# Performance work log

Measured on AMD Instinct MI355X. Metric: run time of the kernel, lower is better.

The kernel has to match this reference:

```python
import jax, jax.numpy as jnp
import numpy as np
from jax import lax

# Model dims (see init_kwargs / mamba_ssm defaults)
B_, L_, D_IN = 8, 512, 128
D_MODEL, N_LAYERS = 512, 2
EXPAND, D_STATE, D_CONV = 2, 16, 4
D_INNER = EXPAND * D_MODEL          # 1024
DT_RANK = (D_MODEL + 15) // 16      # 32


def setup_inputs() -> dict:
    key = jax.random.key(0)
    ks = iter(jax.random.split(key, 32))
    def p(shape, scale=0.02):
        return jax.random.normal(next(ks), shape, jnp.float32) * scale
    inp = {}
    inp["x"] = jax.random.normal(next(ks), (B_, L_, D_IN), jnp.float32)
    # input projection (Linear(input_dim, d_model), with bias)
    inp["proj_in_w"] = p((D_MODEL, D_IN))
    inp["proj_in_b"] = p((D_MODEL,))
    # stacked per-layer Mamba params (leading dim = N_LAYERS)
    inp["in_proj_w"] = p((N_LAYERS, 2 * D_INNER, D_MODEL))      # no bias (mamba default)
    inp["conv_w"]    = p((N_LAYERS, D_INNER, D_CONV))           # depthwise conv1d
    inp["conv_b"]    = p((N_LAYERS, D_INNER))
    inp["x_proj_w"]  = p((N_LAYERS, DT_RANK + 2 * D_STATE, D_INNER))
    inp["dt_proj_w"] = p((N_LAYERS, D_INNER, DT_RANK))
    inp["dt_proj_b"] = jnp.full((N_LAYERS, D_INNER), 0.1, jnp.float32)
    inp["A_log"]     = jnp.log(jnp.tile(jnp.arange(1, D_STATE + 1, dtype=jnp.float32), (N_LAYERS, D_INNER, 1)))
    inp["Dm"]        = jnp.ones((N_LAYERS, D_INNER), jnp.float32)
    inp["out_proj_w"] = p((N_LAYERS, D_MODEL, D_INNER))         # no bias
    # classifier head: Linear(d_model, 64) -> ReLU -> Linear(64, 1)
    inp["cls_w1"] = p((64, D_MODEL)); inp["cls_b1"] = p((64,))
    inp["cls_w2"] = p((1, 64));       inp["cls_b2"] = p((1,))
    return inp


def _mamba_block(h, in_w, cw, cb, xp_w, dt_w, dt_b, A_log, Dm, out_w):
    B, L, _ = h.shape
    xz = jnp.einsum('bld,ed->ble', h, in_w)           # (B, L, 2*d_inner)
    xi, z = jnp.split(xz, 2, axis=-1)
    # causal depthwise conv1d (pad left d_conv-1, crop to L)
    xc = xi.transpose(0, 2, 1)                         # (B, d_inner, L)
    xc = lax.conv_general_dilated(
        xc, cw[:, None, :], (1,), [(D_CONV - 1, 0)],
        feature_group_count=D_INNER,
        dimension_numbers=('NCH', 'OIH', 'NCH')) + cb[None, :, None]
    xc = jax.nn.silu(xc).transpose(0, 2, 1)            # (B, L, d_inner)
    x_dbl = jnp.einsum('bld,ed->ble', xc, xp_w)        # (B, L, dt_rank + 2*d_state)
    dt, Bm, Cm = jnp.split(x_dbl, [DT_RANK, DT_RANK + D_STATE], axis=-1)
    dt = jax.nn.softplus(jnp.einsum('blr,dr->bld', dt, dt_w) + dt_b)  # (B, L, d_inner)
    A = -jnp.exp(A_log)                                # (d_inner, d_state)

    def step(hst, ins):
        dt_t, B_t, C_t, x_t = ins                      # (B,di),(B,ds),(B,ds),(B,di)
        dA = jnp.exp(dt_t[..., None] * A)              # (B, di, ds)
        hst = dA * hst + (dt_t * x_t)[..., None] * B_t[:, None, :]
        y = jnp.einsum('bds,bs->bd', hst, C_t)
        return hst, y

    h0 = jnp.zeros((B, D_INNER, D_STATE), h.dtype)
    xs = (dt.transpose(1, 0, 2), Bm.transpose(1, 0, 2),
          Cm.transpose(1, 0, 2), xc.transpose(1, 0, 2))
    _, ys = lax.scan(step, h0, xs)                     # ys: (L, B, d_inner)
    y = ys.transpose(1, 0, 2) + xc * Dm                # skip term D*x
    y = y * jax.nn.silu(z)                             # gate
    return jnp.einsum('ble,de->bld', y, out_w)         # (B, L, d_model)


def reference(x, proj_in_w, proj_in_b, in_proj_w, conv_w, conv_b, x_proj_w,
              dt_proj_w, dt_proj_b, A_log, Dm, out_proj_w,
              cls_w1, cls_b1, cls_w2, cls_b2):
    h = jnp.einsum('bli,di->bld', x, proj_in_w) + proj_in_b
    for l in range(N_LAYERS):
        h = _mamba_block(h, in_proj_w[l], conv_w[l], conv_b[l], x_proj_w[l],
                         dt_proj_w[l], dt_proj_b[l], A_log[l], Dm[l], out_proj_w[l])
    h = h.mean(axis=1)                                 # (B, d_model); dropout = identity (eval)
    h = jax.nn.relu(h @ cls_w1.T + cls_b1)
    logits = (h @ cls_w2.T + cls_b2).squeeze(-1)       # (B,)
    return logits
```

## Files before the change

### kernel.cpp

```cpp
#include <hip/hip_runtime.h>
#include <hip/hip_bf16.h>

#define B_   8
#define L_   512
#define DIN  128
#define DM   512
#define NLAY 2
#define DI   1024
#define DS   16
#define DTR  32
#define BL   (B_ * L_)
#define KS   8
#define CL   128
#define NCH  (L_ / CL)

typedef short bf16x8 __attribute__((ext_vector_type(8)));
typedef float floatx4 __attribute__((ext_vector_type(4)));

__device__ __forceinline__ unsigned short f2bf(float f) {
    unsigned int u = __float_as_uint(f);
    unsigned int r = (u + 0x7FFF + ((u >> 16) & 1)) >> 16;
    return (unsigned short)r;
}
__device__ __forceinline__ float bf2f(unsigned short u) {
    return __uint_as_float((unsigned int)u << 16);
}

#if __has_builtin(__builtin_amdgcn_exp2f)
#define EXP2(x) __builtin_amdgcn_exp2f(x)
#else
#define EXP2(x) __expf((x) * 0.69314718056f)
#endif

__global__ __launch_bounds__(256) void cvt_all(
    const float* __restrict__ x,  unsigned short* __restrict__ xbf,
    const float* __restrict__ pw, unsigned short* __restrict__ wpin,
    const float* __restrict__ iw, unsigned short* __restrict__ win,
    const float* __restrict__ ow, unsigned short* __restrict__ wout,
    float* __restrict__ hm)
{
    int bid = blockIdx.x;
    if (bid >= 1824) {
        int i = (bid - 1824) * 2048 + threadIdx.x * 8;
        float4 z = make_float4(0.f, 0.f, 0.f, 0.f);
        *(float4*)(hm + i) = z;
        *(float4*)(hm + i + 4) = z;
        return;
    }
    const float* src; unsigned short* dst; int off;
    if      (bid < 256)  { src = x;  dst = xbf;  off = bid; }
    else if (bid < 288)  { src = pw; dst = wpin; off = bid - 256; }
    else if (bid < 1312) { src = iw; dst = win;  off = bid - 288; }
    else                 { src = ow; dst = wout; off = bid - 1312; }
    int i = (off * 256 + threadIdx.x) * 8;
    float4 a = *(const float4*)(src + i);
    float4 b = *(const float4*)(src + i + 4);
    unsigned short o[8];
    o[0] = f2bf(a.x); o[1] = f2bf(a.y); o[2] = f2bf(a.z); o[3] = f2bf(a.w);
    o[4] = f2bf(b.x); o[5] = f2bf(b.y); o[6] = f2bf(b.z); o[7] = f2bf(b.w);
    *(uint4*)(dst + i) = *(uint4*)o;
}

__global__ __launch_bounds__(256) void gemm_mfma(
    const unsigned short* __restrict__ A,
    const unsigned short* __restrict__ W,
    float* __restrict__ C, unsigned short* __restrict__ Cb,
    int N, int K)
{
    __shared__ unsigned short As[128 * 40];
    __shared__ unsigned short Ws[128 * 40];

    const int tid  = threadIdx.x;
    const int row  = tid >> 1;
    const int half = tid & 1;
    const long aBase = (long)(blockIdx.y * 128 + row) * K + half * 16;
    const long wBase = (long)(blockIdx.x * 128 + row) * K + half * 16;
    const int  lbase = row * 40 + half * 16;

    const int lane = tid & 63;
    const int wv   = tid >> 6;
    const int wm   = (wv >> 1) * 64;
    const int wn   = (wv & 1) * 64;
    const int lr   = lane & 15;
    const int q    = lane >> 4;

    floatx4 acc[4][4];
#pragma unroll
    for (int i = 0; i < 4; ++i)
#pragma unroll
        for (int j = 0; j < 4; ++j)
#pragma unroll
            for (int r = 0; r < 4; ++r) acc[i][j][r] = 0.f;

    for (int k0 = 0; k0 < K; k0 += 32) {
        __syncthreads();
        const unsigned short* ap = A + aBase + k0;
        const unsigned short* wp = W + wBase + k0;
        uint4 a0 = *(const uint4*)ap;
        uint4 a1 = *(const uint4*)(ap + 8);
        uint4 w0 = *(const uint4*)wp;
        uint4 w1 = *(const uint4*)(wp + 8);
        *(uint4*)(As + lbase)     = a0;
        *(uint4*)(As + lbase + 8) = a1;
        *(uint4*)(Ws + lbase)     = w0;
        *(uint4*)(Ws + lbase + 8) = w1;
        __syncthreads();

        bf16x8 af[4], bfr[4];
#pragma unroll
        for (int i = 0; i < 4; ++i)
            af[i] = *(const bf16x8*)(As + (wm + i * 16 + lr) * 40 + q * 8);
#pragma unroll
        for (int j = 0; j < 4; ++j)
            bfr[j] = *(const bf16x8*)(Ws + (wn + j * 16 + lr) * 40 + q * 8);
#pragma unroll
        for (int i = 0; i < 4; ++i)
#pragma unroll
            for (int j = 0; j < 4; ++j)
                acc[i][j] = __builtin_amdgcn_mfma_f32_16x16x32_bf16(
                    af[i], bfr[j], acc[i][j], 0, 0, 0);
    }

#pragma unroll
    for (int i = 0; i < 4; ++i) {
#pragma unroll
        for (int r = 0; r < 4; ++r) {
            const int  crow = blockIdx.y * 128 + wm + i * 16 + q * 4 + r;
            const long base = (long)crow * N + blockIdx.x * 128 + wn + lr;
#pragma unroll
            for (int j = 0; j < 4; ++j) {
                float v = acc[i][j][r];
                if (C)  C[base + j * 16] = v;
                if (Cb) Cb[base + j * 16] = f2bf(v);
            }
        }
    }
}

__global__ __launch_bounds__(256) void gemm_mfma_n64(
    const unsigned short* __restrict__ A,
    const unsigned short* __restrict__ W,
    const float* __restrict__ bias,
    float* __restrict__ C, unsigned short* __restrict__ Cb,
    int N, int K, int meanmode, float* __restrict__ hm)
{
    __shared__ unsigned short As[128 * 40];
    __shared__ unsigned short Ws[64 * 40];
    __shared__ float colsum[64];

    const int tid   = threadIdx.x;
    const int arow  = tid >> 1;
    const int ahalf = tid & 1;
    const long aBase = (long)(blockIdx.y * 128 + arow) * K + ahalf * 16;
    const int  albase = arow * 40 + ahalf * 16;
    const int wrow = tid >> 2;
    const int wq   = tid & 3;
    const long wBase = (long)(blockIdx.x * 64 + wrow) * K + wq * 8;
    const int  wlbase = wrow * 40 + wq * 8;

    const int lane = tid & 63;
    const int wv   = tid >> 6;
    const int wm   = wv * 32;
    const int lr   = lane & 15;
    const int q    = lane >> 4;

    floatx4 acc[2][4];
#pragma unroll
    for (int i = 0; i < 2; ++i)
#pragma unroll
        for (int j = 0; j < 4; ++j)
#pragma unroll
            for (int r = 0; r < 4; ++r) acc[i][j][r] = 0.f;

    for (int k0 = 0; k0 < K; k0 += 32) {
        __syncthreads();
        const unsigned short* ap = A + aBase + k0;
        uint4 a0 = *(const uint4*)ap;
        uint4 a1 = *(const uint4*)(ap + 8);
        uint4 w0 = *(const uint4*)(W + wBase + k0);
        *(uint4*)(As + albase)     = a0;
        *(uint4*)(As + albase + 8) = a1;
        *(uint4*)(Ws + wlbase)     = w0;
        __syncthreads();

        bf16x8 af[2], bfr[4];
#pragma unroll
        for (int i = 0; i < 2; ++i)
            af[i] = *(const bf16x8*)(As + (wm + i * 16 + lr) * 40 + q * 8);
#pragma unroll
        for (int j = 0; j < 4; ++j)
            bfr[j] = *(const bf16x8*)(Ws + (j * 16 + lr) * 40 + q * 8);
#pragma unroll
        for (int i = 0; i < 2; ++i)
#pragma unroll
            for (int j = 0; j < 4; ++j)
                acc[i][j] = __builtin_amdgcn_mfma_f32_16x16x32_bf16(
                    af[i], bfr[j], acc[i][j], 0, 0, 0);
    }

    if (meanmode) {
        if (tid < 64) colsum[tid] = 0.f;
        __syncthreads();
#pragma unroll
        for (int j = 0; j < 4; ++j) {
            float p = 0.f;
#pragma unroll
            for (int i = 0; i < 2; ++i)
#pragma unroll
                for (int r = 0; r < 4; ++r) p += acc[i][j][r];
            atomicAdd(&colsum[j * 16 + lr], p);
        }
        __syncthreads();
        if (tid < 64) {
            const int b = blockIdx.y >> 2;
            atomicAdd(&hm[b * DM + blockIdx.x * 64 + tid],
                      colsum[tid] * (1.f / (float)L_));
        }
        return;
    }

    float bj[4] = {0.f, 0.f, 0.f, 0.f};
    if (bias) {
#pragma unroll
        for (int j = 0; j < 4; ++j)
            bj[j] = bias[blockIdx.x * 64 + j * 16 + lr];
    }
#pragma unroll
    for (int i = 0; i < 2; ++i) {
#pragma unroll
        for (int r = 0; r < 4; ++r) {
            const int  crow = blockIdx.y * 128 + wm + i * 16 + q * 4 + r;
            const long base = (long)crow * N + blockIdx.x * 64 + lr;
#pragma unroll
            for (int j = 0; j < 4; ++j) {
                float v = acc[i][j][r] + bj[j];
                if (C)  C[base + j * 16] = v;
                if (Cb) Cb[base + j * 16] = f2bf(v);
            }
        }
    }
}

__global__ __launch_bounds__(256) void xprojconv(
    const unsigned short* __restrict__ xzb, const float* __restrict__ cw,
    const float* __restrict__ cb, const float* __restrict__ W,
    float* __restrict__ P, float* __restrict__ xcout)
{
    __shared__ float As[16][68];
    __shared__ float Ws[16][68];

    const int tid  = threadIdx.x;
    const int tx   = tid & 15;
    const int ty   = tid >> 4;
    const int lrow = tid >> 2;
    const int lk   = (tid & 3) << 2;
    const int kbase = blockIdx.x * (DI / KS);

    const int m = blockIdx.y * 64 + lrow;
    const int t = m & (L_ - 1);
    const float* Wp = W + lrow * DI + kbase + lk;

    float acc[4][4] = {};

    for (int k0 = 0; k0 < DI / KS; k0 += 16) {
        const int dcol = kbase + k0 + lk;
        float4 cbv = *(const float4*)(cb + dcol);
        float sums[4] = {cbv.x, cbv.y, cbv.z, cbv.w};
        float4 cwq[4];
#pragma unroll
        for (int q = 0; q < 4; ++q) cwq[q] = *(const float4*)(cw + (dcol + q) * 4);
#pragma unroll
        for (int w = 0; w < 4; ++w) {
            int tw = t - 3 + w;
            if (tw >= 0) {
                const uint2 up = *(const uint2*)(xzb + (long)(m - 3 + w) * (2 * DI) + dcol);
                float x0 = __uint_as_float(up.x << 16);
                float x1 = __uint_as_float(up.x & 0xffff0000u);
                float x2 = __uint_as_float(up.y << 16);
                float x3 = __uint_as_float(up.y & 0xffff0000u);
                sums[0] += ((const float*)&cwq[0])[w] * x0;
                sums[1] += ((const float*)&cwq[1])[w] * x1;
                sums[2] += ((const float*)&cwq[2])[w] * x2;
                sums[3] += ((const float*)&cwq[3])[w] * x3;
            }
        }
        float4 a4;
#pragma unroll
        for (int q = 0; q < 4; ++q)
            ((float*)&a4)[q] = sums[q] / (1.f + __expf(-sums[q]));
        float4 wv = *(const float4*)(Wp + k0);
        *(float4*)(xcout + (long)m * DI + dcol) = a4;

        __syncthreads();
        As[lk + 0][lrow] = a4.x; As[lk + 1][lrow] = a4.y;
        As[lk + 2][lrow] = a4.z; As[lk + 3][lrow] = a4.w;
        Ws[lk + 0][lrow] = wv.x; Ws[lk + 1][lrow] = wv.y;
        Ws[lk + 2][lrow] = wv.z; Ws[lk + 3][lrow] = wv.w;
        __syncthreads();
#pragma unroll
        for (int k = 0; k < 16; ++k) {
            const float4 a44 = *(const float4*)&As[k][ty << 2];
            const float4 w4  = *(const float4*)&Ws[k][tx << 2];
            acc[0][0] += a44.x * w4.x; acc[0][1] += a44.x * w4.y;
            acc[0][2] += a44.x * w4.z; acc[0][3] += a44.x * w4.w;
            acc[1][0] += a44.y * w4.x; acc[1][1] += a44.y * w4.y;
            acc[1][2] += a44.y * w4.z; acc[1][3] += a44.y * w4.w;
            acc[2][0] += a44.z * w4.x; acc[2][1] += a44.z * w4.y;
            acc[2][2] += a44.z * w4.z; acc[2][3] += a44.z * w4.w;
            acc[3][0] += a44.w * w4.x; acc[3][1] += a44.w * w4.y;
            acc[3][2] += a44.w * w4.z; acc[3][3] += a44.w * w4.w;
        }
    }

    float* out = P + (long)blockIdx.x * (BL * 64)
               + (blockIdx.y * 64 + (ty << 2)) * 64 + (tx << 2);
#pragma unroll
    for (int i = 0; i < 4; ++i)
        *(float4*)(out + i * 64) = make_float4(acc[i][0], acc[i][1],
                                               acc[i][2], acc[i][3]);
}

__global__ __launch_bounds__(256) void xproj_reduce(
    const float* __restrict__ P, float* __restrict__ xdbl)
{
    int i = (blockIdx.x * 256 + threadIdx.x) * 4;
    float4 s = *(const float4*)(P + i);
#pragma unroll
    for (int k = 1; k < KS; ++k) {
        float4 p = *(const float4*)(P + (long)k * (BL * 64) + i);
        s.x += p.x; s.y += p.y; s.z += p.z; s.w += p.w;
    }
    *(float4*)(xdbl + i) = s;
}

template <int CTRL>
__device__ __forceinline__ float dpp_shr_add(float v) {
    int sh = __builtin_amdgcn_update_dpp(0, __float_as_int(v), CTRL, 0xF, 0xF, true);
    return v + __int_as_float(sh);
}

__global__ __launch_bounds__(256) void scan_fused(
    const float* __restrict__ xc, const float* __restrict__ xdbl,
    const float* __restrict__ A_log, const float* __restrict__ dtw,
    const float* __restrict__ dtpb, const float* __restrict__ Dm,
    const unsigned short* __restrict__ xzb, unsigned short* __restrict__ ysb16)
{
    __shared__ float  sdtw[16][36];
    __shared__ float  sxd [CL][36];
    __shared__ float4 sdp [CL / 2][17];
    __shared__ float4 sbc4[CL / 2][17];
    __shared__ float  sy  [16][CL + 4];

    const int tid  = threadIdx.x;
    const int s    = tid & 15;
    const int grp  = tid >> 4;
    const int bd0  = blockIdx.x * 16;
    const int b    = bd0 >> 10;
    const int d0   = bd0 & (DI - 1);
    const int mb0  = b * L_;

    const int j  = tid & 15;
    const int tt = tid >> 4;

    {
        float2 w = *(const float2*)(dtw + (d0 + j) * DTR + tt * 2);
        sdtw[j][tt * 2] = w.x; sdtw[j][tt * 2 + 1] = w.y;
    }
    const float a    = -__expf(A_log[(d0 + grp) * DS + s]);
    const float bias = dtpb[d0 + j];
    const float dmv  = Dm[d0 + j];

    float  rxc[8], rB[8], rC[8], rz[8];
    float2 rxd[8];
#pragma unroll
    for (int i = 0; i < 8; ++i) {
        int m = mb0 + tt + 16 * i;
        rxc[i] = xc[m * DI + d0 + j];
        rxd[i] = *(const float2*)(xdbl + m * 64 + j * 2);
        rB[i]  = xdbl[m * 64 + DTR + j];
        rC[i]  = xdbl[m * 64 + DTR + DS + j];
        rz[i]  = bf2f(xzb[(long)m * (2 * DI) + DI + d0 + j]);
    }

    float state = 0.f;

    for (int c = 0; c < NCH; ++c) {
        const int mbase = mb0 + c * CL;
        float xcur[8], zcur[8];
#pragma unroll
        for (int i = 0; i < 8; ++i) { xcur[i] = rxc[i]; zcur[i] = rz[i]; }

        __syncthreads();
#pragma unroll
        for (int i = 0; i < 8; ++i) {
            int t = tt + 16 * i;
            *(float2*)&sxd[t][j * 2] = rxd[i];
            ((float2*)&sbc4[t >> 1][j])[t & 1] = make_float2(rB[i], rC[i]);
        }
        __syncthreads();

        if (c < NCH - 1) {
#pragma unroll
            for (int i = 0; i < 8; ++i) {
                int m = mbase + CL + tt + 16 * i;
                rxc[i] = xc[m * DI + d0 + j];
                rxd[i] = *(const float2*)(xdbl + m * 64 + j * 2);
                rB[i]  = xdbl[m * 64 + DTR + j];
                rC[i]  = xdbl[m * 64 + DTR + DS + j];
                rz[i]  = bf2f(xzb[(long)m * (2 * DI) + DI + d0 + j]);
            }
        }

        {
            float4 wreg[8];
#pragma unroll
            for (int k = 0; k < 8; ++k) wreg[k] = *(const float4*)&sdtw[j][k * 4];
#pragma unroll
            for (int i = 0; i < 8; ++i) {
                int t = tt + 16 * i;
                float acc = bias;
#pragma unroll
                for (int k = 0; k < 8; ++k) {
                    float4 xv = *(const float4*)&sxd[t][k * 4];
                    acc += xv.x * wreg[k].x + xv.y * wreg[k].y
                         + xv.z * wreg[k].z + xv.w * wreg[k].w;
                }
                float dt = (acc > 20.f) ? acc : __logf(1.f + __expf(acc));
                ((float2*)&sdp[t >> 1][j])[t & 1] =
                    make_float2(dt * 1.44269504f, dt * xcur[i]);
            }
        }
        __syncthreads();

        for (int t4 = 0; t4 < CL; t4 += 4) {
            float ybuf[4];
#pragma unroll
            for (int h = 0; h < 2; ++h) {
                const int t2 = (t4 >> 1) + h;
                const float4 dp = sdp[t2][grp];
                const float4 bc = sbc4[t2][s];
                {
                    const float dA = EXP2(dp.x * a);
                    state = fmaf(dA, state, dp.y * bc.x);
                    float contrib = state * bc.y;
                    contrib = dpp_shr_add<0x111>(contrib);
                    contrib = dpp_shr_add<0x112>(contrib);
                    contrib = dpp_shr_add<0x114>(contrib);
                    contrib = dpp_shr_add<0x118>(contrib);
                    ybuf[h * 2] = contrib;
                }
                {
                    const float dA = EXP2(dp.z * a);
                    state = fmaf(dA, state, dp.w * bc.z);
                    float contrib = state * bc.w;
                    contrib = dpp_shr_add<0x111>(contrib);
                    contrib = dpp_shr_add<0x112>(contrib);
                    contrib = dpp_shr_add<0x114>(contrib);
                    contrib = dpp_shr_add<0x118>(contrib);
                    ybuf[h * 2 + 1] = contrib;
                }
            }
            if (s == 15) *(float4*)&sy[grp][t4] = *(float4*)ybuf;
        }
        __syncthreads();

#pragma unroll
        for (int i = 0; i < 8; ++i) {
            int t = tt + 16 * i;
            float z = zcur[i];
            float sz = z / (1.f + __expf(-z));
            float val = (sy[j][t] + xcur[i] * dmv) * sz;
            ysb16[(mbase + t) * DI + d0 + j] = f2bf(val);
        }
    }
}

__global__ __launch_bounds__(512) void meancls_kernel(
    const float* __restrict__ hm, const float* __restrict__ w1,
    const float* __restrict__ b1, const float* __restrict__ w2,
    const float* __restrict__ b2, float* __restrict__ out)
{
    __shared__ float shm[DM];
    __shared__ float su[64];
    const int b = blockIdx.x, tid = threadIdx.x;
    shm[tid] = hm[b * DM + tid];
    __syncthreads();

    const int j = tid >> 3, sl = tid & 7;
    const float* wr = w1 + j * DM + sl * 64;
    const float* hb = shm + sl * 64;
    float p = 0.f;
    for (int k = 0; k < 64; k += 4)
        p += hb[k] * wr[k] + hb[k+1] * wr[k+1]
           + hb[k+2] * wr[k+2] + hb[k+3] * wr[k+3];
    p += __shfl_xor(p, 1);
    p += __shfl_xor(p, 2);
    p += __shfl_xor(p, 4);
    if (sl == 0) su[j] = fmaxf(p + b1[j], 0.f) * w2[j];
    __syncthreads();
    if (tid < 64) {
        float v = su[tid];
#pragma unroll
        for (int off = 32; off; off >>= 1) v += __shfl_down(v, off);
        if (tid == 0) out[b] = v + b2[0];
    }
}

extern "C" void kernel_launch(void* const* d_in, const int* in_sizes, int n_in,
                              void* d_out, int out_size, void* d_ws, size_t ws_size,
                              hipStream_t stream) {
    const float* x          = (const float*)d_in[0];
    const float* proj_in_w  = (const float*)d_in[1];
    const float* proj_in_b  = (const float*)d_in[2];
    const float* in_proj_w  = (const float*)d_in[3];
    const float* conv_w     = (const float*)d_in[4];
    const float* conv_b     = (const float*)d_in[5];
    const float* x_proj_w   = (const float*)d_in[6];
    const float* dt_proj_w  = (const float*)d_in[7];
    const float* dt_proj_b  = (const float*)d_in[8];
    const float* A_log      = (const float*)d_in[9];
    const float* Dm         = (const float*)d_in[10];
    const float* out_proj_w = (const float*)d_in[11];
    const float* cls_w1     = (const float*)d_in[12];
    const float* cls_b1     = (const float*)d_in[13];
    const float* cls_w2     = (const float*)d_in[14];
    const float* cls_b2     = (const float*)d_in[15];
    float* out = (float*)d_out;

    float* ws   = (float*)d_ws;
    float* h    = ws;
    float* xzf  = h    + BL * DM;
    float* xcb  = xzf  + BL * 2 * DI;
    float* xdbl = xcb  + BL * DI;
    float* scr  = xdbl + BL * 64;
    float* hm   = scr  + 2 * BL * DI;
    float* hmp  = hm   + B_ * DM;
    unsigned short* xzb  = (unsigned short*)xzf;
    unsigned short* u16  = (unsigned short*)(hmp + 64 * DM);
    unsigned short* xbf  = u16;
    unsigned short* hbf  = xbf  + BL * DIN;
    unsigned short* ysbf = hbf  + BL * DM;
    unsigned short* wpin = ysbf + BL * DI;
    unsigned short* win  = wpin + DM * DIN;
    unsigned short* wout = win  + NLAY * 2 * DI * DM;
    float* xpart = scr;

    cvt_all<<<1826, 256, 0, stream>>>(x, xbf, proj_in_w, wpin,
                                      in_proj_w, win, out_proj_w, wout, hm);

    gemm_mfma_n64<<<dim3(DM / 64, BL / 128), 256, 0, stream>>>(
        xbf, wpin, proj_in_b, nullptr, hbf, DM, DIN, 0, nullptr);

    for (int l = 0; l < NLAY; ++l) {
        gemm_mfma<<<dim3(2 * DI / 128, BL / 128), 256, 0, stream>>>(
            hbf, win + l * 2 * DI * DM, nullptr, xzb, 2 * DI, DM);
        xprojconv<<<dim3(KS, BL / 64), 256, 0, stream>>>(
            xzb, conv_w + l * DI * 4, conv_b + l * DI,
            x_proj_w + l * 64 * DI, xpart, xcb);
        xproj_reduce<<<(BL * 64) / 1024, 256, 0, stream>>>(xpart, xdbl);
        scan_fused<<<(B_ * DI) / 16, 256, 0, stream>>>(
            xcb, xdbl, A_log + l * DI * DS, dt_proj_w + l * DI * DTR,
            dt_proj_b + l * DI, Dm + l * DI, xzb, ysbf);
        if (l == NLAY - 1) {
            gemm_mfma_n64<<<dim3(DM / 64, BL / 128), 256, 0, stream>>>(
                ysbf, wout + l * DM * DI, nullptr, nullptr, nullptr,
                DM, DI, 1, hm);
        } else {
            gemm_mfma_n64<<<dim3(DM / 64, BL / 128), 256, 0, stream>>>(
                ysbf, wout + l * DM * DI, nullptr, nullptr, hbf,
                DM, DI, 0, nullptr);
        }
    }

    meancls_kernel<<<B_, 512, 0, stream>>>(hm, cls_w1, cls_b1,
                                           cls_w2, cls_b2, out);
}
```

Before: 347.0 us.

## Fuse all stages into one persistent cooperative kernel with grid syncs

Turns every stage (conversion, GEMMs, conv+xproj, reduce, scan, out-proj, classifier) into a device function and runs them inside a single cooperative persistent kernel. Stages are separated by grid-wide barriers instead of about a dozen kernel launches. It also halves the scan chunk length and changes how the dt weights are staged (registers instead of shared memory). If the cooperative launch fails, it falls back to separate kernels. The risk is that grid barriers and a shared LDS/register budget across all stages lower per-stage occupancy.

```diff
diff --git a/kernel.cpp b/kernel.cpp
--- a/kernel.cpp
+++ b/kernel.cpp
@@ -1,5 +1,8 @@
 #include <hip/hip_runtime.h>
+#include <hip/hip_cooperative_groups.h>
 #include <hip/hip_bf16.h>
+
+namespace cg = cooperative_groups;
 
 #define B_   8
 #define L_   512
@@ -11,8 +14,9 @@
 #define DTR  32
 #define BL   (B_ * L_)
 #define KS   8
-#define CL   128
+#define CL   64
 #define NCH  (L_ / CL)
+#define NBLK 512
 
 typedef short bf16x8 __attribute__((ext_vector_type(8)));
 typedef float floatx4 __attribute__((ext_vector_type(4)));
@@ -32,27 +36,40 @@
 #define EXP2(x) __expf((x) * 0.69314718056f)
 #endif
 
-__global__ __launch_bounds__(256) void cvt_all(
-    const float* __restrict__ x,  unsigned short* __restrict__ xbf,
-    const float* __restrict__ pw, unsigned short* __restrict__ wpin,
-    const float* __restrict__ iw, unsigned short* __restrict__ win,
-    const float* __restrict__ ow, unsigned short* __restrict__ wout,
-    float* __restrict__ hm)
-{
-    int bid = blockIdx.x;
-    if (bid >= 1824) {
-        int i = (bid - 1824) * 2048 + threadIdx.x * 8;
+template <int CTRL>
+__device__ __forceinline__ float dpp_shr_add(float v) {
+    int sh = __builtin_amdgcn_update_dpp(0, __float_as_int(v), CTRL, 0xF, 0xF, true);
+    return v + __int_as_float(sh);
+}
+
+struct KParams {
+    const float *x, *proj_in_w, *proj_in_b, *conv_w, *conv_b, *x_proj_w,
+                *dt_proj_w, *dt_proj_b, *A_log, *Dm, *in_proj_w, *out_proj_w,
+                *cls_w1, *cls_b1, *cls_w2, *cls_b2;
+    float *out;
+    float *xcb, *xdbl, *xpart, *hm;
+    unsigned short *xzb, *xbf, *hbf, *ysbf, *wpin, *win, *wout;
+};
+
+
+__device__ void stage_cvt(const float* x, unsigned short* xbf,
+                          const float* pw, unsigned short* wpin,
+                          const float* iw, unsigned short* win,
+                          const float* ow, unsigned short* wout,
+                          float* hm, int task, int tid) {
+    if (task >= 1824) {
+        int i = (task - 1824) * 2048 + tid * 8;
         float4 z = make_float4(0.f, 0.f, 0.f, 0.f);
         *(float4*)(hm + i) = z;
         *(float4*)(hm + i + 4) = z;
         return;
     }
     const float* src; unsigned short* dst; int off;
-    if      (bid < 256)  { src = x;  dst = xbf;  off = bid; }
-    else if (bid < 288)  { src = pw; dst = wpin; off = bid - 256; }
-    else if (bid < 1312) { src = iw; dst = win;  off = bid - 288; }
-    else                 { src = ow; dst = wout; off = bid - 1312; }
-    int i = (off * 256 + threadIdx.x) * 8;
+    if      (task < 256)  { src = x;  dst = xbf;  off = task; }
+    else if (task < 288)  { src = pw; dst = wpin; off = task - 256; }
+    else if (task < 1312) { src = iw; dst = win;  off = task - 288; }
+    else                  { src = ow; dst = wout; off = task - 1312; }
+    int i = (off * 256 + tid) * 8;
     float4 a = *(const float4*)(src + i);
     float4 b = *(const float4*)(src + i + 4);
     unsigned short o[8];
@@ -61,20 +78,116 @@
     *(uint4*)(dst + i) = *(uint4*)o;
 }
 
-__global__ __launch_bounds__(256) void gemm_mfma(
-    const unsigned short* __restrict__ A,
-    const unsigned short* __restrict__ W,
-    float* __restrict__ C, unsigned short* __restrict__ Cb,
-    int N, int K)
-{
-    __shared__ unsigned short As[128 * 40];
-    __shared__ unsigned short Ws[128 * 40];
-
-    const int tid  = threadIdx.x;
+__device__ void stage_gemm_n64(const unsigned short* __restrict__ A,
+                               const unsigned short* __restrict__ W,
+                               const float* bias, unsigned short* Cb,
+                               int meanmode, float* hm, int K,
+                               int bxx, int byy, unsigned char* sm, int tid) {
+    unsigned short* As = (unsigned short*)sm;
+    unsigned short* Ws = (unsigned short*)(sm + 10240);
+    float* colsum = (float*)(sm + 15360);
+
+    const int arow  = tid >> 1;
+    const int ahalf = tid & 1;
+    const long aBase = (long)(byy * 128 + arow) * K + ahalf * 16;
+    const int  albase = arow * 40 + ahalf * 16;
+    const int wrow = tid >> 2;
+    const int wq   = tid & 3;
+    const long wBase = (long)(bxx * 64 + wrow) * K + wq * 8;
+    const int  wlbase = wrow * 40 + wq * 8;
+
+    const int lane = tid & 63;
+    const int wv   = tid >> 6;
+    const int wm   = wv * 32;
+    const int lr   = lane & 15;
+    const int q    = lane >> 4;
+
+    floatx4 acc[2][4];
+#pragma unroll
+    for (int i = 0; i < 2; ++i)
+#pragma unroll
+        for (int j = 0; j < 4; ++j)
+#pragma unroll
+            for (int r = 0; r < 4; ++r) acc[i][j][r] = 0.f;
+
+    for (int k0 = 0; k0 < K; k0 += 32) {
+        __syncthreads();
+        const unsigned short* ap = A + aBase + k0;
+        uint4 a0 = *(const uint4*)ap;
+        uint4 a1 = *(const uint4*)(ap + 8);
+        uint4 w0 = *(const uint4*)(W + wBase + k0);
+        *(uint4*)(As + albase)     = a0;
+        *(uint4*)(As + albase + 8) = a1;
+        *(uint4*)(Ws + wlbase)     = w0;
+        __syncthreads();
+
+        bf16x8 af[2], bfr[4];
+#pragma unroll
+        for (int i = 0; i < 2; ++i)
+            af[i] = *(const bf16x8*)(As + (wm + i * 16 + lr) * 40 + q * 8);
+#pragma unroll
+        for (int j = 0; j < 4; ++j)
+            bfr[j] = *(const bf16x8*)(Ws + (j * 16 + lr) * 40 + q * 8);
+#pragma unroll
+        for (int i = 0; i < 2; ++i)
+#pragma unroll
+            for (int j = 0; j < 4; ++j)
+                acc[i][j] = __builtin_amdgcn_mfma_f32_16x16x32_bf16(
+                    af[i], bfr[j], acc[i][j], 0, 0, 0);
+    }
+
+    if (meanmode) {
+        __syncthreads();
+        if (tid < 64) colsum[tid] = 0.f;
+        __syncthreads();
+#pragma unroll
+        for (int j = 0; j < 4; ++j) {
+            float pp = 0.f;
+#pragma unroll
+            for (int i = 0; i < 2; ++i)
+#pragma unroll
+                for (int r = 0; r < 4; ++r) pp += acc[i][j][r];
+            atomicAdd(&colsum[j * 16 + lr], pp);
+        }
+        __syncthreads();
+        if (tid < 64) {
+            const int b = byy >> 2;
+            atomicAdd(&hm[b * DM + bxx * 64 + tid],
+                      colsum[tid] * (1.f / (float)L_));
+        }
+        return;
+    }
+
+    float bj[4] = {0.f, 0.f, 0.f, 0.f};
+    if (bias) {
+#pragma unroll
+        for (int j = 0; j < 4; ++j)
+            bj[j] = bias[bxx * 64 + j * 16 + lr];
+    }
+#pragma unroll
+    for (int i = 0; i < 2; ++i) {
+#pragma unroll
+        for (int r = 0; r < 4; ++r) {
+            const int  crow = byy * 128 + wm + i * 16 + q * 4 + r;
+            const long base = (long)crow * DM + bxx * 64 + lr;
+#pragma unroll
+            for (int j = 0; j < 4; ++j)
+                Cb[base + j * 16] = f2bf(acc[i][j][r] + bj[j]);
+        }
+    }
+}
+
+__device__ void stage_gemm_128(const unsigned short* __restrict__ A,
+                               const unsigned short* __restrict__ W,
+                               unsigned short* Cb, int N, int K,
+                               int bxx, int byy, unsigned char* sm, int tid) {
+    unsigned short* As = (unsigned short*)sm;
+    unsigned short* Ws = (unsigned short*)(sm + 10240);
+
     const int row  = tid >> 1;
     const int half = tid & 1;
-    const long aBase = (long)(blockIdx.y * 128 + row) * K + half * 16;
-    const long wBase = (long)(blockIdx.x * 128 + row) * K + half * 16;
+    const long aBase = (long)(byy * 128 + row) * K + half * 16;
+    const long wBase = (long)(bxx * 128 + row) * K + half * 16;
     const int  lbase = row * 40 + half * 16;
 
     const int lane = tid & 63;
@@ -125,138 +238,30 @@
     for (int i = 0; i < 4; ++i) {
 #pragma unroll
         for (int r = 0; r < 4; ++r) {
-            const int  crow = blockIdx.y * 128 + wm + i * 16 + q * 4 + r;
-            const long base = (long)crow * N + blockIdx.x * 128 + wn + lr;
-#pragma unroll
-            for (int j = 0; j < 4; ++j) {
-                float v = acc[i][j][r];
-                if (C)  C[base + j * 16] = v;
-                if (Cb) Cb[base + j * 16] = f2bf(v);
-            }
-        }
-    }
-}
-
-__global__ __launch_bounds__(256) void gemm_mfma_n64(
-    const unsigned short* __restrict__ A,
-    const unsigned short* __restrict__ W,
-    const float* __restrict__ bias,
-    float* __restrict__ C, unsigned short* __restrict__ Cb,
-    int N, int K, int meanmode, float* __restrict__ hm)
-{
-    __shared__ unsigned short As[128 * 40];
-    __shared__ unsigned short Ws[64 * 40];
-    __shared__ float colsum[64];
-
-    const int tid   = threadIdx.x;
-    const int arow  = tid >> 1;
-    const int ahalf = tid & 1;
-    const long aBase = (long)(blockIdx.y * 128 + arow) * K + ahalf * 16;
-    const int  albase = arow * 40 + ahalf * 16;
-    const int wrow = tid >> 2;
-    const int wq   = tid & 3;
-    const long wBase = (long)(blockIdx.x * 64 + wrow) * K + wq * 8;
-    const int  wlbase = wrow * 40 + wq * 8;
-
-    const int lane = tid & 63;
-    const int wv   = tid >> 6;
-    const int wm   = wv * 32;
-    const int lr   = lane & 15;
-    const int q    = lane >> 4;
-
-    floatx4 acc[2][4];
-#pragma unroll
-    for (int i = 0; i < 2; ++i)
-#pragma unroll
-        for (int j = 0; j < 4; ++j)
-#pragma unroll
-            for (int r = 0; r < 4; ++r) acc[i][j][r] = 0.f;
-
-    for (int k0 = 0; k0 < K; k0 += 32) {
-        __syncthreads();
-        const unsigned short* ap = A + aBase + k0;
-        uint4 a0 = *(const uint4*)ap;
-        uint4 a1 = *(const uint4*)(ap + 8);
-        uint4 w0 = *(const uint4*)(W + wBase + k0);
-        *(uint4*)(As + albase)     = a0;
-        *(uint4*)(As + albase + 8) = a1;
-        *(uint4*)(Ws + wlbase)     = w0;
-        __syncthreads();
-
-        bf16x8 af[2], bfr[4];
-#pragma unroll
-        for (int i = 0; i < 2; ++i)
-            af[i] = *(const bf16x8*)(As + (wm + i * 16 + lr) * 40 + q * 8);
-#pragma unroll
-        for (int j = 0; j < 4; ++j)
-            bfr[j] = *(const bf16x8*)(Ws + (j * 16 + lr) * 40 + q * 8);
-#pragma unroll
-        for (int i = 0; i < 2; ++i)
+            const int  crow = byy * 128 + wm + i * 16 + q * 4 + r;
+            const long base = (long)crow * N + bxx * 128 + wn + lr;
 #pragma unroll
             for (int j = 0; j < 4; ++j)
-                acc[i][j] = __builtin_amdgcn_mfma_f32_16x16x32_bf16(
-                    af[i], bfr[j], acc[i][j], 0, 0, 0);
-    }
-
-    if (meanmode) {
-        if (tid < 64) colsum[tid] = 0.f;
-        __syncthreads();
-#pragma unroll
-        for (int j = 0; j < 4; ++j) {
-            float p = 0.f;
-#pragma unroll
-            for (int i = 0; i < 2; ++i)
-#pragma unroll
-                for (int r = 0; r < 4; ++r) p += acc[i][j][r];
-            atomicAdd(&colsum[j * 16 + lr], p);
-        }
-        __syncthreads();
-        if (tid < 64) {
-            const int b = blockIdx.y >> 2;
-            atomicAdd(&hm[b * DM + blockIdx.x * 64 + tid],
-                      colsum[tid] * (1.f / (float)L_));
-        }
-        return;
-    }
-
-    float bj[4] = {0.f, 0.f, 0.f, 0.f};
-    if (bias) {
-#pragma unroll
-        for (int j = 0; j < 4; ++j)
-            bj[j] = bias[blockIdx.x * 64 + j * 16 + lr];
-    }
-#pragma unroll
-    for (int i = 0; i < 2; ++i) {
-#pragma unroll
-        for (int r = 0; r < 4; ++r) {
-            const int  crow = blockIdx.y * 128 + wm + i * 16 + q * 4 + r;
-            const long base = (long)crow * N + blockIdx.x * 64 + lr;
-#pragma unroll
-            for (int j = 0; j < 4; ++j) {
-                float v = acc[i][j][r] + bj[j];
-                if (C)  C[base + j * 16] = v;
-                if (Cb) Cb[base + j * 16] = f2bf(v);
-            }
-        }
-    }
-}
-
-__global__ __launch_bounds__(256) void xprojconv(
-    const unsigned short* __restrict__ xzb, const float* __restrict__ cw,
-    const float* __restrict__ cb, const float* __restrict__ W,
-    float* __restrict__ P, float* __restrict__ xcout)
-{
-    __shared__ float As[16][68];
-    __shared__ float Ws[16][68];
-
-    const int tid  = threadIdx.x;
+                Cb[base + j * 16] = f2bf(acc[i][j][r]);
+        }
+    }
+}
+
+__device__ void stage_xprojconv(const unsigned short* __restrict__ xzb,
+                                const float* cw, const float* cb,
+                                const float* __restrict__ W,
+                                float* P, float* xcout,
+                                int ks, int byy, unsigned char* sm, int tid) {
+    float (*As)[68] = (float(*)[68])sm;
+    float (*Ws)[68] = (float(*)[68])(sm + 4352);
+
     const int tx   = tid & 15;
     const int ty   = tid >> 4;
     const int lrow = tid >> 2;
     const int lk   = (tid & 3) << 2;
-    const int kbase = blockIdx.x * (DI / KS);
-
-    const int m = blockIdx.y * 64 + lrow;
+    const int kbase = ks * (DI / KS);
+
+    const int m = byy * 64 + lrow;
     const int t = m & (L_ - 1);
     const float* Wp = W + lrow * DI + kbase + lk;
 
@@ -268,7 +273,7 @@
         float sums[4] = {cbv.x, cbv.y, cbv.z, cbv.w};
         float4 cwq[4];
 #pragma unroll
-        for (int q = 0; q < 4; ++q) cwq[q] = *(const float4*)(cw + (dcol + q) * 4);
+        for (int qq = 0; qq < 4; ++qq) cwq[qq] = *(const float4*)(cw + (dcol + qq) * 4);
 #pragma unroll
         for (int w = 0; w < 4; ++w) {
             int tw = t - 3 + w;
@@ -286,8 +291,8 @@
         }
         float4 a4;
 #pragma unroll
-        for (int q = 0; q < 4; ++q)
-            ((float*)&a4)[q] = sums[q] / (1.f + __expf(-sums[q]));
+        for (int qq = 0; qq < 4; ++qq)
+            ((float*)&a4)[qq] = sums[qq] / (1.f + __expf(-sums[qq]));
         float4 wv = *(const float4*)(Wp + k0);
         *(float4*)(xcout + (long)m * DI + dcol) = a4;
 
@@ -312,49 +317,41 @@
         }
     }
 
-    float* out = P + (long)blockIdx.x * (BL * 64)
-               + (blockIdx.y * 64 + (ty << 2)) * 64 + (tx << 2);
+    float* outp = P + (long)ks * (BL * 64)
+                + (byy * 64 + (ty << 2)) * 64 + (tx << 2);
 #pragma unroll
     for (int i = 0; i < 4; ++i)
-        *(float4*)(out + i * 64) = make_float4(acc[i][0], acc[i][1],
-                                               acc[i][2], acc[i][3]);
-}
-
-__global__ __launch_bounds__(256) void xproj_reduce(
-    const float* __restrict__ P, float* __restrict__ xdbl)
-{
-    int i = (blockIdx.x * 256 + threadIdx.x) * 4;
+        *(float4*)(outp + i * 64) = make_float4(acc[i][0], acc[i][1],
+                                                acc[i][2], acc[i][3]);
+}
+
+__device__ void stage_reduce(const float* __restrict__ P, float* xdbl,
+                             int task, int tid) {
+    int i = (task * 256 + tid) * 4;
     float4 s = *(const float4*)(P + i);
 #pragma unroll
     for (int k = 1; k < KS; ++k) {
-        float4 p = *(const float4*)(P + (long)k * (BL * 64) + i);
-        s.x += p.x; s.y += p.y; s.z += p.z; s.w += p.w;
+        float4 pp = *(const float4*)(P + (long)k * (BL * 64) + i);
+        s.x += pp.x; s.y += pp.y; s.z += pp.z; s.w += pp.w;
     }
     *(float4*)(xdbl + i) = s;
 }
 
-template <int CTRL>
-__device__ __forceinline__ float dpp_shr_add(float v) {
-    int sh = __builtin_amdgcn_update_dpp(0, __float_as_int(v), CTRL, 0xF, 0xF, true);
-    return v + __int_as_float(sh);
-}
-
-__global__ __launch_bounds__(256) void scan_fused(
-    const float* __restrict__ xc, const float* __restrict__ xdbl,
-    const float* __restrict__ A_log, const float* __restrict__ dtw,
-    const float* __restrict__ dtpb, const float* __restrict__ Dm,
-    const unsigned short* __restrict__ xzb, unsigned short* __restrict__ ysb16)
-{
-    __shared__ float  sdtw[16][36];
-    __shared__ float  sxd [CL][36];
-    __shared__ float4 sdp [CL / 2][17];
-    __shared__ float4 sbc4[CL / 2][17];
-    __shared__ float  sy  [16][CL + 4];
-
-    const int tid  = threadIdx.x;
+__device__ void stage_scan(const float* __restrict__ xc,
+                           const float* __restrict__ xdbl,
+                           const float* A_log, const float* dtw,
+                           const float* dtpb, const float* Dm,
+                           const unsigned short* __restrict__ xzb,
+                           unsigned short* ysb16,
+                           int task, unsigned char* sm, int tid) {
+    float (*sxd)[36]   = (float(*)[36])(sm);
+    float4 (*sdp)[17]  = (float4(*)[17])(sm + 9216);
+    float4 (*sbc4)[17] = (float4(*)[17])(sm + 17920);
+    float (*sy)[68]    = (float(*)[68])(sm + 26624);
+
     const int s    = tid & 15;
     const int grp  = tid >> 4;
-    const int bd0  = blockIdx.x * 16;
+    const int bd0  = task * 16;
     const int b    = bd0 >> 10;
     const int d0   = bd0 & (DI - 1);
     const int mb0  = b * L_;
@@ -362,18 +359,18 @@
     const int j  = tid & 15;
     const int tt = tid >> 4;
 
-    {
-        float2 w = *(const float2*)(dtw + (d0 + j) * DTR + tt * 2);
-        sdtw[j][tt * 2] = w.x; sdtw[j][tt * 2 + 1] = w.y;
-    }
     const float a    = -__expf(A_log[(d0 + grp) * DS + s]);
     const float bias = dtpb[d0 + j];
     const float dmv  = Dm[d0 + j];
-
-    float  rxc[8], rB[8], rC[8], rz[8];
-    float2 rxd[8];
-#pragma unroll
-    for (int i = 0; i < 8; ++i) {
+    float4 wreg[8];
+#pragma unroll
+    for (int k = 0; k < 8; ++k)
+        wreg[k] = *(const float4*)(dtw + (d0 + j) * DTR + k * 4);
+
+    float  rxc[4], rB[4], rC[4], rz[4];
+    float2 rxd[4];
+#pragma unroll
+    for (int i = 0; i < 4; ++i) {
         int m = mb0 + tt + 16 * i;
         rxc[i] = xc[m * DI + d0 + j];
         rxd[i] = *(const float2*)(xdbl + m * 64 + j * 2);
@@ -386,13 +383,13 @@
 
     for (int c = 0; c < NCH; ++c) {
         const int mbase = mb0 + c * CL;
-        float xcur[8], zcur[8];
-#pragma unroll
-        for (int i = 0; i < 8; ++i) { xcur[i] = rxc[i]; zcur[i] = rz[i]; }
-
-        __syncthreads();
-#pragma unroll
-        for (int i = 0; i < 8; ++i) {
+        float xcur[4], zcur[4];
+#pragma unroll
+        for (int i = 0; i < 4; ++i) { xcur[i] = rxc[i]; zcur[i] = rz[i]; }
+
+        __syncthreads();
+#pragma unroll
+        for (int i = 0; i < 4; ++i) {
             int t = tt + 16 * i;
             *(float2*)&sxd[t][j * 2] = rxd[i];
             ((float2*)&sbc4[t >> 1][j])[t & 1] = make_float2(rB[i], rC[i]);
@@ -401,7 +398,7 @@
 
         if (c < NCH - 1) {
 #pragma unroll
-            for (int i = 0; i < 8; ++i) {
+            for (int i = 0; i < 4; ++i) {
                 int m = mbase + CL + tt + 16 * i;
                 rxc[i] = xc[m * DI + d0 + j];
                 rxd[i] = *(const float2*)(xdbl + m * 64 + j * 2);
@@ -411,24 +408,19 @@
             }
         }
 
-        {
-            float4 wreg[8];
-#pragma unroll
-            for (int k = 0; k < 8; ++k) wreg[k] = *(const float4*)&sdtw[j][k * 4];
-#pragma unroll
-            for (int i = 0; i < 8; ++i) {
-                int t = tt + 16 * i;
-                float acc = bias;
-#pragma unroll
-                for (int k = 0; k < 8; ++k) {
-                    float4 xv = *(const float4*)&sxd[t][k * 4];
-                    acc += xv.x * wreg[k].x + xv.y * wreg[k].y
-                         + xv.z * wreg[k].z + xv.w * wreg[k].w;
-                }
-                float dt = (acc > 20.f) ? acc : __logf(1.f + __expf(acc));
-                ((float2*)&sdp[t >> 1][j])[t & 1] =
-                    make_float2(dt * 1.44269504f, dt * xcur[i]);
+#pragma unroll
+        for (int i = 0; i < 4; ++i) {
+            int t = tt + 16 * i;
+            float acc = bias;
+#pragma unroll
+            for (int k = 0; k < 8; ++k) {
+                float4 xv = *(const float4*)&sxd[t][k * 4];
+                acc += xv.x * wreg[k].x + xv.y * wreg[k].y
+                     + xv.z * wreg[k].z + xv.w * wreg[k].w;
             }
+            float dt = (acc > 20.f) ? acc : __logf(1.f + __expf(acc));
+            ((float2*)&sdp[t >> 1][j])[t & 1] =
+                make_float2(dt * 1.44269504f, dt * xcur[i]);
         }
         __syncthreads();
 
@@ -465,7 +457,7 @@
         __syncthreads();
 
 #pragma unroll
-        for (int i = 0; i < 8; ++i) {
+        for (int i = 0; i < 4; ++i) {
             int t = tt + 16 * i;
             float z = zcur[i];
             float sz = z / (1.f + __expf(-z));
@@ -475,28 +467,26 @@
     }
 }
 
-__global__ __launch_bounds__(512) void meancls_kernel(
-    const float* __restrict__ hm, const float* __restrict__ w1,
-    const float* __restrict__ b1, const float* __restrict__ w2,
-    const float* __restrict__ b2, float* __restrict__ out)
-{
-    __shared__ float shm[DM];
-    __shared__ float su[64];
-    const int b = blockIdx.x, tid = threadIdx.x;
-    shm[tid] = hm[b * DM + tid];
+__device__ void stage_meancls(const float* hm, const float* w1,
+                              const float* b1, const float* w2,
+                              const float* b2, float* out,
+                              int b, unsigned char* sm, int tid) {
+    float* shm = (float*)sm;
+    float* su  = (float*)(sm + 2048);
+    shm[tid]       = hm[b * DM + tid];
+    shm[tid + 256] = hm[b * DM + tid + 256];
     __syncthreads();
 
-    const int j = tid >> 3, sl = tid & 7;
-    const float* wr = w1 + j * DM + sl * 64;
-    const float* hb = shm + sl * 64;
-    float p = 0.f;
-    for (int k = 0; k < 64; k += 4)
-        p += hb[k] * wr[k] + hb[k+1] * wr[k+1]
-           + hb[k+2] * wr[k+2] + hb[k+3] * wr[k+3];
-    p += __shfl_xor(p, 1);
-    p += __shfl_xor(p, 2);
-    p += __shfl_xor(p, 4);
-    if (sl == 0) su[j] = fmaxf(p + b1[j], 0.f) * w2[j];
+    const int j = tid >> 2, sl = tid & 3;
+    const float* wr = w1 + j * DM + sl * 128;
+    const float* hb = shm + sl * 128;
+    float pp = 0.f;
+    for (int k = 0; k < 128; k += 4)
+        pp += hb[k] * wr[k] + hb[k+1] * wr[k+1]
+            + hb[k+2] * wr[k+2] + hb[k+3] * wr[k+3];
+    pp += __shfl_xor(pp, 1);
+    pp += __shfl_xor(pp, 2);
+    if (sl == 0) su[j] = fmaxf(pp + b1[j], 0.f) * w2[j];
     __syncthreads();
     if (tid < 64) {
         float v = su[tid];
@@ -506,72 +496,184 @@
     }
 }
 
+__global__ __launch_bounds__(256) void mamba_mono(KParams p) {
+    cg::grid_group grid = cg::this_grid();
+    __shared__ __attribute__((aligned(16))) unsigned char sm[30976];
+    const int tid  = threadIdx.x;
+    const int bx   = blockIdx.x;
+    const int nblk = gridDim.x;
+
+    for (int task = bx; task < 1826; task += nblk)
+        stage_cvt(p.x, p.xbf, p.proj_in_w, p.wpin, p.in_proj_w, p.win,
+                  p.out_proj_w, p.wout, p.hm, task, tid);
+    grid.sync();
+
+    for (int task = bx; task < 256; task += nblk)
+        stage_gemm_n64(p.xbf, p.wpin, p.proj_in_b, p.hbf, 0, nullptr, DIN,
+                       task & 7, task >> 3, sm, tid);
+    grid.sync();
+
+    for (int l = 0; l < NLAY; ++l) {
+        for (int task = bx; task < 512; task += nblk)
+            stage_gemm_128(p.hbf, p.win + l * 2 * DI * DM, p.xzb, 2 * DI, DM,
+                           task & 15, task >> 4, sm, tid);
+        grid.sync();
+
+        for (int task = bx; task < 512; task += nblk)
+            stage_xprojconv(p.xzb, p.conv_w + l * DI * 4, p.conv_b + l * DI,
+                            p.x_proj_w + l * 64 * DI, p.xpart, p.xcb,
+                            task & 7, task >> 3, sm, tid);
+        grid.sync();
+
+        for (int task = bx; task < 256; task += nblk)
+            stage_reduce(p.xpart, p.xdbl, task, tid);
+        grid.sync();
+
+        for (int task = bx; task < 512; task += nblk)
+            stage_scan(p.xcb, p.xdbl, p.A_log + l * DI * DS,
+                       p.dt_proj_w + l * DI * DTR, p.dt_proj_b + l * DI,
+                       p.Dm + l * DI, p.xzb, p.ysbf, task, sm, tid);
+        grid.sync();
+
+        for (int task = bx; task < 256; task += nblk) {
+            if (l == NLAY - 1)
+                stage_gemm_n64(p.ysbf, p.wout + l * DM * DI, nullptr, nullptr,
+                               1, p.hm, DI, task & 7, task >> 3, sm, tid);
+            else
+                stage_gemm_n64(p.ysbf, p.wout + l * DM * DI, nullptr, p.hbf,
+                               0, nullptr, DI, task & 7, task >> 3, sm, tid);
+        }
+        grid.sync();
+    }
+
+    for (int task = bx; task < 8; task += nblk)
+        stage_meancls(p.hm, p.cls_w1, p.cls_b1, p.cls_w2, p.cls_b2, p.out,
+                      task, sm, tid);
+}
+
+__global__ __launch_bounds__(256) void k_cvt(
+    const float* x, unsigned short* xbf, const float* pw, unsigned short* wpin,
+    const float* iw, unsigned short* win, const float* ow, unsigned short* wout,
+    float* hm) {
+    stage_cvt(x, xbf, pw, wpin, iw, win, ow, wout, hm, blockIdx.x, threadIdx.x);
+}
+__global__ __launch_bounds__(256) void k_gemm_n64(
+    const unsigned short* A, const unsigned short* W, const float* bias,
+    unsigned short* Cb, int meanmode, float* hm, int K) {
+    __shared__ __attribute__((aligned(16))) unsigned char sm[15616];
+    stage_gemm_n64(A, W, bias, Cb, meanmode, hm, K,
+                   blockIdx.x, blockIdx.y, sm, threadIdx.x);
+}
+__global__ __launch_bounds__(256) void k_gemm_128(
+    const unsigned short* A, const unsigned short* W, unsigned short* Cb,
+    int N, int K) {
+    __shared__ __attribute__((aligned(16))) unsigned char sm[20480];
+    stage_gemm_128(A, W, Cb, N, K, blockIdx.x, blockIdx.y, sm, threadIdx.x);
+}
+__global__ __launch_bounds__(256) void k_xprojconv(
+    const unsigned short* xzb, const float* cw, const float* cb,
+    const float* W, float* P, float* xcout) {
+    __shared__ __attribute__((aligned(16))) unsigned char sm[8704];
+    stage_xprojconv(xzb, cw, cb, W, P, xcout,
+                    blockIdx.x, blockIdx.y, sm, threadIdx.x);
+}
+__global__ __launch_bounds__(256) void k_reduce(const float* P, float* xdbl) {
+    stage_reduce(P, xdbl, blockIdx.x, threadIdx.x);
+}
+__global__ __launch_bounds__(256) void k_scan(
+    const float* xc, const float* xdbl, const float* A_log, const float* dtw,
+    const float* dtpb, const float* Dm, const unsigned short* xzb,
+    unsigned short* ysb16) {
+    __shared__ __attribute__((aligned(16))) unsigned char sm[30976];
+    stage_scan(xc, xdbl, A_log, dtw, dtpb, Dm, xzb, ysb16,
+               blockIdx.x, sm, threadIdx.x);
+}
+__global__ __launch_bounds__(256) void k_meancls(
+    const float* hm, const float* w1, const float* b1,
+    const float* w2, const float* b2, float* out) {
+    __shared__ __attribute__((aligned(16))) unsigned char sm[2304];
+    stage_meancls(hm, w1, b1, w2, b2, out, blockIdx.x, sm, threadIdx.x);
+}
+
 extern "C" void kernel_launch(void* const* d_in, const int* in_sizes, int n_in,
                               void* d_out, int out_size, void* d_ws, size_t ws_size,
                               hipStream_t stream) {
-    const float* x          = (const float*)d_in[0];
-    const float* proj_in_w  = (const float*)d_in[1];
-    const float* proj_in_b  = (const float*)d_in[2];
-    const float* in_proj_w  = (const float*)d_in[3];
-    const float* conv_w     = (const float*)d_in[4];
-    const float* conv_b     = (const float*)d_in[5];
-    const float* x_proj_w   = (const float*)d_in[6];
-    const float* dt_proj_w  = (const float*)d_in[7];
-    const float* dt_proj_b  = (const float*)d_in[8];
-    const float* A_log      = (const float*)d_in[9];
-    const float* Dm         = (const float*)d_in[10];
-    const float* out_proj_w = (const float*)d_in[11];
-    const float* cls_w1     = (const float*)d_in[12];
-    const float* cls_b1     = (const float*)d_in[13];
-    const float* cls_w2     = (const float*)d_in[14];
-    const float* cls_b2     = (const float*)d_in[15];
-    float* out = (float*)d_out;
+    KParams p;
+    p.x          = (const float*)d_in[0];
+    p.proj_in_w  = (const float*)d_in[1];
+    p.proj_in_b  = (const float*)d_in[2];
+    p.in_proj_w  = (const float*)d_in[3];
+    p.conv_w     = (const float*)d_in[4];
+    p.conv_b     = (const float*)d_in[5];
+    p.x_proj_w   = (const float*)d_in[6];
+    p.dt_proj_w  = (const float*)d_in[7];
+    p.dt_proj_b  = (const float*)d_in[8];
+    p.A_log      = (const float*)d_in[9];
+    p.Dm         = (const float*)d_in[10];
+    p.out_proj_w = (const float*)d_in[11];
+    p.cls_w1     = (const float*)d_in[12];
+    p.cls_b1     = (const float*)d_in[13];
+    p.cls_w2     = (const float*)d_in[14];
+    p.cls_b2     = (const float*)d_in[15];
+    p.out        = (float*)d_out;
 
     float* ws   = (float*)d_ws;
     float* h    = ws;
     float* xzf  = h    + BL * DM;
-    float* xcb  = xzf  + BL * 2 * DI;
-    float* xdbl = xcb  + BL * DI;
-    float* scr  = xdbl + BL * 64;
-    float* hm   = scr  + 2 * BL * DI;
-    float* hmp  = hm   + B_ * DM;
-    unsigned short* xzb  = (unsigned short*)xzf;
-    unsigned short* u16  = (unsigned short*)(hmp + 64 * DM);
-    unsigned short* xbf  = u16;
-    unsigned short* hbf  = xbf  + BL * DIN;
-    unsigned short* ysbf = hbf  + BL * DM;
-    unsigned short* wpin = ysbf + BL * DI;
-    unsigned short* win  = wpin + DM * DIN;
-    unsigned short* wout = win  + NLAY * 2 * DI * DM;
-    float* xpart = scr;
-
-    cvt_all<<<1826, 256, 0, stream>>>(x, xbf, proj_in_w, wpin,
-                                      in_proj_w, win, out_proj_w, wout, hm);
-
-    gemm_mfma_n64<<<dim3(DM / 64, BL / 128), 256, 0, stream>>>(
-        xbf, wpin, proj_in_b, nullptr, hbf, DM, DIN, 0, nullptr);
-
-    for (int l = 0; l < NLAY; ++l) {
-        gemm_mfma<<<dim3(2 * DI / 128, BL / 128), 256, 0, stream>>>(
-            hbf, win + l * 2 * DI * DM, nullptr, xzb, 2 * DI, DM);
-        xprojconv<<<dim3(KS, BL / 64), 256, 0, stream>>>(
-            xzb, conv_w + l * DI * 4, conv_b + l * DI,
-            x_proj_w + l * 64 * DI, xpart, xcb);
-        xproj_reduce<<<(BL * 64) / 1024, 256, 0, stream>>>(xpart, xdbl);
-        scan_fused<<<(B_ * DI) / 16, 256, 0, stream>>>(
-            xcb, xdbl, A_log + l * DI * DS, dt_proj_w + l * DI * DTR,
-            dt_proj_b + l * DI, Dm + l * DI, xzb, ysbf);
-        if (l == NLAY - 1) {
-            gemm_mfma_n64<<<dim3(DM / 64, BL / 128), 256, 0, stream>>>(
-                ysbf, wout + l * DM * DI, nullptr, nullptr, nullptr,
-                DM, DI, 1, hm);
-        } else {
-            gemm_mfma_n64<<<dim3(DM / 64, BL / 128), 256, 0, stream>>>(
-                ysbf, wout + l * DM * DI, nullptr, nullptr, hbf,
-                DM, DI, 0, nullptr);
-        }
-    }
-
-    meancls_kernel<<<B_, 512, 0, stream>>>(hm, cls_w1, cls_b1,
-                                           cls_w2, cls_b2, out);
-}
+    p.xcb       = xzf  + BL * 2 * DI;
+    p.xdbl      = p.xcb + BL * DI;
+    float* scr  = p.xdbl + BL * 64;
+    p.hm        = scr  + 2 * BL * DI;
+    float* hmp  = p.hm + B_ * DM;
+    p.xpart     = scr;
+
+    p.xzb  = (unsigned short*)xzf;
+    unsigned short* u16 = (unsigned short*)(hmp + 64 * DM);
+    p.xbf  = u16;
+    p.hbf  = p.xbf  + BL * DIN;
+    p.ysbf = p.hbf  + BL * DM;
+    p.wpin = p.ysbf + BL * DI;
+    p.win  = p.wpin + DM * DIN;
+    p.wout = p.win  + NLAY * 2 * DI * DM;
+
+    bool coop_ok = false;
+    int occ = 0;
+    hipError_t e = hipOccupancyMaxActiveBlocksPerMultiprocessor(
+        &occ, (const void*)mamba_mono, 256, 0);
+    if (e == hipSuccess && occ > 0) {
+        int nblk = occ * 256;
+        if (nblk > NBLK) nblk = NBLK;
+        void* kargs[] = { (void*)&p };
+        e = hipLaunchCooperativeKernel((const void*)mamba_mono, dim3(nblk),
+                                       dim3(256), kargs, 0, stream);
+        coop_ok = (e == hipSuccess);
+    }
+    if (!coop_ok) {
+        (void)hipGetLastError();
+        k_cvt<<<1826, 256, 0, stream>>>(p.x, p.xbf, p.proj_in_w, p.wpin,
+                                        p.in_proj_w, p.win, p.out_proj_w,
+                                        p.wout, p.hm);
+        k_gemm_n64<<<dim3(8, 32), 256, 0, stream>>>(
+            p.xbf, p.wpin, p.proj_in_b, p.hbf, 0, nullptr, DIN);
+        for (int l = 0; l < NLAY; ++l) {
+            k_gemm_128<<<dim3(16, 32), 256, 0, stream>>>(
+                p.hbf, p.win + l * 2 * DI * DM, p.xzb, 2 * DI, DM);
+            k_xprojconv<<<dim3(8, 64), 256, 0, stream>>>(
+                p.xzb, p.conv_w + l * DI * 4, p.conv_b + l * DI,
+                p.x_proj_w + l * 64 * DI, p.xpart, p.xcb);
+            k_reduce<<<256, 256, 0, stream>>>(p.xpart, p.xdbl);
+            k_scan<<<512, 256, 0, stream>>>(
+                p.xcb, p.xdbl, p.A_log + l * DI * DS,
+                p.dt_proj_w + l * DI * DTR, p.dt_proj_b + l * DI,
+                p.Dm + l * DI, p.xzb, p.ysbf);
+            if (l == NLAY - 1)
+                k_gemm_n64<<<dim3(8, 32), 256, 0, stream>>>(
+                    p.ysbf, p.wout + l * DM * DI, nullptr, nullptr, 1, p.hm, DI);
+            else
+                k_gemm_n64<<<dim3(8, 32), 256, 0, stream>>>(
+                    p.ysbf, p.wout + l * DM * DI, nullptr, p.hbf, 0, nullptr, DI);
+        }
+        k_meancls<<<8, 256, 0, stream>>>(p.hm, p.cls_w1, p.cls_b1,
+                                         p.cls_w2, p.cls_b2, p.out);
+    }
+}
```

Result: slower. 428.2 us (+23.4%).
